# Kernel optimization log

Hardware: AMD Instinct MI355X
Metric: run time of the kernel (lower is better)

The kernel has to match this reference:

```python
import jax, jax.numpy as jnp
import numpy as np

BN_EPS = 1e-5


def _bn(x, gamma, beta):
    # training-mode BatchNorm1d: biased batch stats over the edge/batch axis
    mean = jnp.mean(x, axis=0, keepdims=True)
    var = jnp.mean((x - mean) ** 2, axis=0, keepdims=True)
    return (x - mean) * jax.lax.rsqrt(var + BN_EPS) * gamma + beta


def setup_inputs() -> dict:
    key = jax.random.key(0)
    ks = jax.random.split(key, 20)
    N, E = 20000, 300000
    in_drug, in_prot, hidden = 256, 512, 256
    h2 = 2 * hidden

    def u(k, shape, fan_in):
        b = 1.0 / np.sqrt(fan_in)
        return jax.random.uniform(k, shape, jnp.float32, -b, b)

    return {
        "x_drug": jax.random.normal(ks[0], (N, in_drug), jnp.float32),
        "x_prot": jax.random.normal(ks[1], (N, in_prot), jnp.float32),
        "edge_index": jax.random.randint(ks[2], (2, E), 0, N, jnp.int64),
        "W_src": u(ks[3], (hidden, in_drug), in_drug),
        "W_dst": u(ks[4], (hidden, in_prot), in_prot),
        "W_gate": u(ks[5], (h2, h2), h2),
        "b_gate": u(ks[6], (h2,), h2),
        "W1": u(ks[7], (hidden, h2), h2),
        "b1": u(ks[8], (hidden,), h2),
        "g1": jnp.ones((hidden,), jnp.float32),
        "be1": jnp.zeros((hidden,), jnp.float32),
        "W2": u(ks[9], (hidden, hidden), hidden),
        "b2": u(ks[10], (hidden,), hidden),
        "g2": jnp.ones((hidden,), jnp.float32),
        "be2": jnp.zeros((hidden,), jnp.float32),
        "W3": u(ks[11], (1, hidden), hidden),
        "b3": u(ks[12], (1,), hidden),
        "W_bil": u(ks[13], (1, hidden, hidden), hidden),
        "b_bil": u(ks[14], (1,), hidden),
    }


def reference(x_drug, x_prot, edge_index, W_src, W_dst, W_gate, b_gate,
              W1, b1, g1, be1, W2, b2, g2, be2, W3, b3, W_bil, b_bil):
    src, dst = edge_index[0], edge_index[1]
    h_src = x_drug[src] @ W_src.T            # [E, H]
    h_dst = x_prot[dst] @ W_dst.T            # [E, H]
    h_cat = jnp.concatenate([h_src, h_dst], axis=1)  # [E, 2H]
    gate = jax.nn.sigmoid(h_cat @ W_gate.T + b_gate)
    h = gate * h_cat
    # MLP (dropout is identity here)
    h1 = jax.nn.relu(_bn(h @ W1.T + b1, g1, be1))
    h2_ = jax.nn.relu(_bn(h1 @ W2.T + b2, g2, be2))
    mlp_score = (h2_ @ W3.T + b3).reshape(-1)
    # Bilinear: out_ek = sum_ij h_src_ei W_kij h_dst_ej + b_k
    bil_score = (jnp.einsum("ei,kij,ej->ek", h_src, W_bil, h_dst) + b_bil).reshape(-1)
    return mlp_score + bil_score
```

## Files before the change

### kernel.cpp

```cpp
#include <hip/hip_runtime.h>
#include <hip/hip_bf16.h>

typedef unsigned short u16;
typedef unsigned int u32;
typedef __attribute__((ext_vector_type(8))) short bf16x8;
typedef __attribute__((ext_vector_type(8))) unsigned short us8;
typedef __attribute__((ext_vector_type(4))) float f32x4;


__device__ __forceinline__ float b2f(u16 u) {
    union { unsigned u32v; float f; } x; x.u32v = ((unsigned)u) << 16; return x.f;
}
__device__ __forceinline__ u16 f2b(float f) {
    __hip_bfloat16 h = __float2bfloat16(f);
    u16 r; __builtin_memcpy(&r, &h, 2); return r;
}

struct CvtSeg { const float* in; u16* out; int n4; };
struct CvtArr { CvtSeg s[4]; int tot4; };
__global__ __launch_bounds__(256) void cvt_fused(CvtArr ca) {
    int i = blockIdx.x * 256 + threadIdx.x;
    if (i >= ca.tot4) return;
    int k = 0, off = i;
#pragma unroll
    for (int q = 0; q < 4; ++q) {
        if (off < ca.s[q].n4) { k = q; break; }
        off -= ca.s[q].n4;
    }
    float4 v = ((const float4*)ca.s[k].in)[off];
    ushort4 o; o.x = f2b(v.x); o.y = f2b(v.y); o.z = f2b(v.z); o.w = f2b(v.w);
    ((ushort4*)ca.s[k].out)[off] = o;
}

__global__ __launch_bounds__(256) void repack_swz(const float* __restrict__ W,
                                                  u16* __restrict__ out,
                                                  int total, int kbits) {
    int idx = blockIdx.x * 256 + threadIdx.x;
    if (idx >= total) return;
    const int n = idx >> kbits;
    const int k = idx & ((1 << kbits) - 1);
    const int ks = k >> 6, ke = k & 63;
    const int j = ke ^ ((n & 7) << 3);
    out[(((ks << 8) + n) << 6) + j] = f2b(W[idx]);
}

__global__ __launch_bounds__(256) void hist_kernel(const int* __restrict__ ei,
                                                   int E, u32* __restrict__ hist) {
    int e = blockIdx.x * 256 + threadIdx.x;
    if (e < E) atomicAdd(&hist[ei[E + e]], 1u);
}

__global__ __launch_bounds__(256) void scan_kernel(const u32* __restrict__ hist,
                                                   u32* __restrict__ cursor, int n) {
    __shared__ u32 part[256];
    const int t = threadIdx.x;
    const int chunk = (n + 255) / 256;
    const int lo = t * chunk, hi = min(lo + chunk, n);
    u32 s = 0;
    for (int i = lo; i < hi; ++i) s += hist[i];
    part[t] = s;
    __syncthreads();
    for (int off = 1; off < 256; off <<= 1) {
        u32 v = (t >= off) ? part[t - off] : 0u;
        __syncthreads();
        part[t] += v;
        __syncthreads();
    }
    u32 base = (t == 0) ? 0u : part[t - 1];
    for (int i = lo; i < hi; ++i) {
        cursor[i] = base;
        base += hist[i];
    }
}

__global__ __launch_bounds__(256) void scatter_kernel(const int* __restrict__ ei,
                                                      int E, u32* __restrict__ cursor,
                                                      int2* __restrict__ sd,
                                                      int* __restrict__ pe) {
    int e = blockIdx.x * 256 + threadIdx.x;
    if (e >= E) return;
    const int d = ei[E + e];
    const u32 pos = atomicAdd(&cursor[d], 1u);
    sd[pos] = make_int2(ei[e], d);
    pe[pos] = e;
}

struct GDesc {
    const void* A; int lda; int a_f32;
    const u16* W; int ldb;
    u16* C; int ldc;
    int K;
    const float* bias;
};
template <int NY> struct GDescArr { GDesc d[NY]; };

template <int NY>
__global__ __launch_bounds__(256, 2) void mfma_node(GDescArr<NY> da, int M)
{
    const GDesc dd = da.d[blockIdx.y];
    __shared__ u16 As[2][128][40];
    __shared__ u16 Bs[2][256][40];
    const int t = threadIdx.x;
    const int row0 = blockIdx.x * 128;
    const int arow = t >> 1, aks = (t & 1) * 16;
    const int agr = min(row0 + arow, M - 1);
    const int w = t >> 6, lane = t & 63;
    const int wr = w >> 1, wc = w & 1;
    const int lrow = lane & 15, lkg = lane >> 4;
    const int NIT = dd.K >> 5;

    f32x4 acc[4][8] = {};
    us8 ar[2], br[4];
    float4 fr[4];

    auto load_regs = [&](int it) {
        const int k0 = it << 5;
        if (dd.a_f32) {
            const float* ap = (const float*)dd.A + (size_t)agr * dd.lda + k0 + aks;
#pragma unroll
            for (int q = 0; q < 4; ++q) fr[q] = *(const float4*)(ap + q * 4);
        } else {
            const u16* ap = (const u16*)dd.A + (size_t)agr * dd.lda + k0 + aks;
            ar[0] = *(const us8*)ap; ar[1] = *(const us8*)(ap + 8);
        }
        const u16* wp = dd.W + (size_t)t * dd.ldb + k0;
#pragma unroll
        for (int q = 0; q < 4; ++q) br[q] = *(const us8*)(wp + q * 8);
    };
    auto proc_write = [&](int b) {
        if (dd.a_f32) {
#pragma unroll
            for (int q = 0; q < 2; ++q) {
                us8 o;
                const float fq[8] = {fr[q*2].x, fr[q*2].y, fr[q*2].z, fr[q*2].w,
                                     fr[q*2+1].x, fr[q*2+1].y, fr[q*2+1].z, fr[q*2+1].w};
#pragma unroll
                for (int j = 0; j < 8; ++j) o[j] = f2b(fq[j]);
                *(us8*)&As[b][arow][aks + q * 8] = o;
            }
        } else {
            *(us8*)&As[b][arow][aks] = ar[0];
            *(us8*)&As[b][arow][aks + 8] = ar[1];
        }
#pragma unroll
        for (int q = 0; q < 4; ++q) *(us8*)&Bs[b][t][q * 8] = br[q];
    };
    auto do_mfma = [&](int b) {
        bf16x8 af[4];
#pragma unroll
        for (int mi = 0; mi < 4; ++mi)
            af[mi] = *(const bf16x8*)&As[b][wr * 64 + mi * 16 + lrow][lkg * 8];
#pragma unroll
        for (int ni = 0; ni < 8; ++ni) {
            bf16x8 bfr = *(const bf16x8*)&Bs[b][wc * 128 + ni * 16 + lrow][lkg * 8];
#pragma unroll
            for (int mi = 0; mi < 4; ++mi)
                acc[mi][ni] = __builtin_amdgcn_mfma_f32_16x16x32_bf16(
                    af[mi], bfr, acc[mi][ni], 0, 0, 0);
        }
    };

    load_regs(0); proc_write(0); __syncthreads();
    for (int it = 0; it < NIT; ++it) {
        const int cur = it & 1;
        if (it + 1 < NIT) load_regs(it + 1);
        do_mfma(cur);
        if (it + 1 < NIT) proc_write(cur ^ 1);
        __syncthreads();
    }

#pragma unroll
    for (int ni = 0; ni < 8; ++ni) {
        const int gcol = wc * 128 + ni * 16 + lrow;
        const float bv = dd.bias ? dd.bias[gcol] : 0.f;
#pragma unroll
        for (int mi = 0; mi < 4; ++mi) {
            f32x4 v = acc[mi][ni];
#pragma unroll
            for (int j = 0; j < 4; ++j) {
                const int grow = row0 + wr * 64 + mi * 16 + lkg * 4 + j;
                if (grow < M) dd.C[(size_t)grow * dd.ldc + gcol] = f2b(v[j] + bv);
            }
        }
    }
}

#define OP_GATE   1
#define OP_BNRELU 2

template <int AOP>
__global__ __launch_bounds__(256) void mfma_edge(
    const u16* __restrict__ Ain,
    const u16* __restrict__ Wb, int K,
    u16* __restrict__ C, int E,
    const int2* __restrict__ sd,
    const u16* __restrict__ Gs, const u16* __restrict__ Gd,
    const u16* __restrict__ Hs, const u16* __restrict__ Hd,
    const u16* __restrict__ Bd, const float* __restrict__ b_bil,
    float* __restrict__ bil,
    const float* __restrict__ scaleK, const float* __restrict__ shiftK,
    float* __restrict__ sums)
{
    __shared__ u16 As[64][72];
    __shared__ u16 Bs[256 * 64];
    __shared__ float wsum[2][256];

    const int t = threadIdx.x;
    const int row0 = blockIdx.x * 64;
    const int arow = t >> 2;
    const int aks  = (t & 3) * 16;
    const int agr = min(row0 + arow, E - 1);

    int s_ = 0, d_ = 0;
    if constexpr (AOP == OP_GATE) {
        int2 p = sd[agr]; s_ = p.x; d_ = p.y;
    }

    const int lane = t & 63;
    const int w = t >> 6;
    const int lrow = lane & 15, lkg = lane >> 4;
    const int NKS = K >> 6;

    f32x4 acc[4][4] = {};
    float bdot = 0.f;
    us8 aw0, aw1;

    auto loadA = [&](int ks) {
        const int k = ks * 64 + aks;
        if constexpr (AOP == OP_GATE) {
            us8 gs0 = *(const us8*)(Gs + (size_t)s_ * 512 + k);
            us8 gs1 = *(const us8*)(Gs + (size_t)s_ * 512 + k + 8);
            us8 gd0 = *(const us8*)(Gd + (size_t)d_ * 512 + k);
            us8 gd1 = *(const us8*)(Gd + (size_t)d_ * 512 + k + 8);
            const u16* hp = (ks < 4) ? (Hs + (size_t)s_ * 256 + k)
                                     : (Hd + (size_t)d_ * 256 + k - 256);
            us8 h0 = *(const us8*)hp, h1 = *(const us8*)(hp + 8);
#pragma unroll
            for (int j = 0; j < 8; ++j) {
                const float x0 = b2f(gs0[j]) + b2f(gd0[j]);
                const float x1 = b2f(gs1[j]) + b2f(gd1[j]);
                const float r0 = __builtin_amdgcn_rcpf(1.f + __expf(-x0));
                const float r1 = __builtin_amdgcn_rcpf(1.f + __expf(-x1));
                aw0[j] = f2b(b2f(h0[j]) * r0);
                aw1[j] = f2b(b2f(h1[j]) * r1);
            }
            if (ks < 4) {
                us8 bd0 = *(const us8*)(Bd + (size_t)d_ * 256 + k);
                us8 bd1 = *(const us8*)(Bd + (size_t)d_ * 256 + k + 8);
#pragma unroll
                for (int j = 0; j < 8; ++j) {
                    bdot = fmaf(b2f(h0[j]), b2f(bd0[j]), bdot);
                    bdot = fmaf(b2f(h1[j]), b2f(bd1[j]), bdot);
                }
            }
        } else {
            us8 a0 = *(const us8*)(Ain + (size_t)agr * 256 + k);
            us8 a1 = *(const us8*)(Ain + (size_t)agr * 256 + k + 8);
            float4 c0 = *(const float4*)(scaleK + k);
            float4 c1 = *(const float4*)(scaleK + k + 4);
            float4 c2 = *(const float4*)(scaleK + k + 8);
            float4 c3 = *(const float4*)(scaleK + k + 12);
            float4 h0 = *(const float4*)(shiftK + k);
            float4 h1 = *(const float4*)(shiftK + k + 4);
            float4 h2 = *(const float4*)(shiftK + k + 8);
            float4 h3 = *(const float4*)(shiftK + k + 12);
            const float scq[16] = {c0.x,c0.y,c0.z,c0.w, c1.x,c1.y,c1.z,c1.w,
                                   c2.x,c2.y,c2.z,c2.w, c3.x,c3.y,c3.z,c3.w};
            const float shq[16] = {h0.x,h0.y,h0.z,h0.w, h1.x,h1.y,h1.z,h1.w,
                                   h2.x,h2.y,h2.z,h2.w, h3.x,h3.y,h3.z,h3.w};
#pragma unroll
            for (int j = 0; j < 8; ++j) {
                aw0[j] = f2b(fmaxf(fmaf(b2f(a0[j]), scq[j],     shq[j]),     0.f));
                aw1[j] = f2b(fmaxf(fmaf(b2f(a1[j]), scq[8 + j], shq[8 + j]), 0.f));
            }
        }
    };
    auto writeA = [&]() {
        *(us8*)&As[arow][aks]     = aw0;
        *(us8*)&As[arow][aks + 8] = aw1;
    };
    auto gloadB = [&](int ks) {
        const char* g = (const char*)(Wb + ((size_t)ks << 14)) + w * 8192 + lane * 16;
        char* l = (char*)Bs + w * 8192;
#pragma unroll
        for (int q = 0; q < 8; ++q)
            __builtin_amdgcn_global_load_lds(
                (const __attribute__((address_space(1))) unsigned int*)(g + q * 1024),
                (__attribute__((address_space(3))) unsigned int*)(l + q * 1024),
                16, 0, 0);
    };
    auto mfma_slab = [&]() {
#pragma unroll
        for (int kk = 0; kk < 64; kk += 32) {
            bf16x8 af[4], bf[4];
#pragma unroll
            for (int mi = 0; mi < 4; ++mi)
                af[mi] = *(const bf16x8*)&As[mi * 16 + lrow][kk + lkg * 8];
#pragma unroll
            for (int ni = 0; ni < 4; ++ni) {
                const int r = w * 64 + ni * 16 + lrow;
                bf[ni] = *(const bf16x8*)&Bs[r * 64 + ((kk + lkg * 8) ^ ((r & 7) << 3))];
            }
#pragma unroll
            for (int ni = 0; ni < 4; ++ni)
#pragma unroll
                for (int mi = 0; mi < 4; ++mi)
                    acc[mi][ni] = __builtin_amdgcn_mfma_f32_16x16x32_bf16(
                        af[mi], bf[ni], acc[mi][ni], 0, 0, 0);
        }
    };

    gloadB(0); loadA(0);
    for (int ks = 0; ks < NKS; ++ks) {
        writeA();
        __syncthreads();
        if (ks + 1 < NKS) loadA(ks + 1);
        mfma_slab();
        __syncthreads();
        if (ks + 1 < NKS) gloadB(ks + 1);
    }

    if constexpr (AOP == OP_GATE) {
        bdot += __shfl_xor(bdot, 1, 64);
        bdot += __shfl_xor(bdot, 2, 64);
        if ((t & 3) == 0 && row0 + arow < E)
            bil[row0 + arow] = bdot + b_bil[0];
    }

#pragma unroll
    for (int ni = 0; ni < 4; ++ni) {
        const int gcol = w * 64 + ni * 16 + lrow;
        float s = 0.f, ss = 0.f;
#pragma unroll
        for (int mi = 0; mi < 4; ++mi) {
            f32x4 v = acc[mi][ni];
#pragma unroll
            for (int j = 0; j < 4; ++j) {
                const int grow = row0 + mi * 16 + lkg * 4 + j;
                const float x = v[j];
                if (grow < E) {
                    C[(size_t)grow * 256 + gcol] = f2b(x);
                    s += x; ss = fmaf(x, x, ss);
                }
            }
        }
        s  += __shfl_xor(s, 16, 64);  s  += __shfl_xor(s, 32, 64);
        ss += __shfl_xor(ss, 16, 64); ss += __shfl_xor(ss, 32, 64);
        if (lkg == 0) { wsum[0][gcol] = s; wsum[1][gcol] = ss; }
    }
    __syncthreads();
    atomicAdd(&sums[t],       wsum[0][t]);
    atomicAdd(&sums[256 + t], wsum[1][t]);
}

__global__ void finalize_kernel(
    const float* __restrict__ sums, const float* __restrict__ g,
    const float* __restrict__ be, int M,
    float* __restrict__ scale, float* __restrict__ shift)
{
    const int c = threadIdx.x;
    const float inv = 1.f / (float)M;
    const float mean = sums[c] * inv;
    const float var  = sums[256 + c] * inv - mean * mean;
    const float sc = g[c] * rsqrtf(var + 1e-5f);
    scale[c] = sc;
    shift[c] = fmaf(-mean, sc, be[c]);
}

__global__ __launch_bounds__(256) void final_kernel(
    const u16* __restrict__ Z2,
    const float* __restrict__ scale2, const float* __restrict__ shift2,
    const float* __restrict__ W3, const float* __restrict__ b3,
    const float* __restrict__ bil, const int* __restrict__ pe,
    float* __restrict__ out, int E)
{
    const int w = threadIdx.x >> 6, lane = threadIdx.x & 63;
    const int e = blockIdx.x * 4 + w;
    if (e >= E) return;
    ushort4 zv = *(const ushort4*)(Z2 + (size_t)e * 256 + lane * 4);
    float4 sc = *(const float4*)(scale2 + lane * 4);
    float4 sh = *(const float4*)(shift2 + lane * 4);
    float4 w3 = *(const float4*)(W3 + lane * 4);
    const u16 zq[4] = {zv.x, zv.y, zv.z, zv.w};
    const float scq[4] = {sc.x, sc.y, sc.z, sc.w};
    const float shq[4] = {sh.x, sh.y, sh.z, sh.w};
    const float wq[4] = {w3.x, w3.y, w3.z, w3.w};
    float acc = 0.f;
#pragma unroll
    for (int i = 0; i < 4; ++i) {
        const float x = fmaxf(fmaf(b2f(zq[i]), scq[i], shq[i]), 0.f);
        acc = fmaf(x, wq[i], acc);
    }
#pragma unroll
    for (int off = 32; off; off >>= 1) acc += __shfl_down(acc, off, 64);
    if (lane == 0) out[pe[e]] = acc + b3[0] + bil[e];
}

extern "C" void kernel_launch(void* const* d_in, const int* in_sizes, int n_in,
                              void* d_out, int out_size, void* d_ws, size_t ws_size,
                              hipStream_t stream)
{
    const float* x_drug = (const float*)d_in[0];
    const float* x_prot = (const float*)d_in[1];
    const int*   ei     = (const int*)d_in[2];
    const float* W_src  = (const float*)d_in[3];
    const float* W_dst  = (const float*)d_in[4];
    const float* W_gate = (const float*)d_in[5];
    const float* b_gate = (const float*)d_in[6];
    const float* W1     = (const float*)d_in[7];
    const float* g1     = (const float*)d_in[9];
    const float* be1    = (const float*)d_in[10];
    const float* W2     = (const float*)d_in[11];
    const float* g2     = (const float*)d_in[13];
    const float* be2    = (const float*)d_in[14];
    const float* W3     = (const float*)d_in[15];
    const float* b3     = (const float*)d_in[16];
    const float* W_bil  = (const float*)d_in[17];
    const float* b_bil  = (const float*)d_in[18];
    float* out = (float*)d_out;

    const int N = in_sizes[0] / 256;
    const int E = in_sizes[2] / 2;

    char* wp_ = (char*)d_ws;
    auto alloc = [&](size_t bytes) {
        char* p = wp_; wp_ += (bytes + 255) & ~(size_t)255; return p;
    };
    u16* Wsrcb  = (u16*)alloc(256 * 256 * 2);
    u16* Wdstb  = (u16*)alloc(256 * 512 * 2);
    u16* Wgateb = (u16*)alloc(512 * 512 * 2);
    u16* Wbilb  = (u16*)alloc(256 * 256 * 2);
    u16* W1s    = (u16*)alloc(256 * 512 * 2);
    u16* W2s    = (u16*)alloc(256 * 256 * 2);
    u16* Hs     = (u16*)alloc((size_t)N * 256 * 2);
    u16* Hd     = (u16*)alloc((size_t)N * 256 * 2);
    u16* Gs     = (u16*)alloc((size_t)N * 512 * 2);
    u16* Gd     = (u16*)alloc((size_t)N * 512 * 2);
    u16* Bd     = (u16*)alloc((size_t)N * 256 * 2);
    u16* z      = (u16*)alloc((size_t)E * 256 * 2);
    float* bil  = (float*)alloc((size_t)E * 4);
    u32*  hist  = (u32*)alloc((size_t)N * 4);
    u32*  cursor= (u32*)alloc((size_t)N * 4);
    int2* sd    = (int2*)alloc((size_t)E * 8);
    int*  pe    = (int*)alloc((size_t)E * 4);
    float* sums   = (float*)alloc(1024 * 4);
    float* scale1 = (float*)alloc(256 * 4);
    float* shift1 = (float*)alloc(256 * 4);
    float* scale2 = (float*)alloc(256 * 4);
    float* shift2 = (float*)alloc(256 * 4);

    hipMemsetAsync(sums, 0, 1024 * 4, stream);
    hipMemsetAsync(hist, 0, (size_t)N * 4, stream);

    hist_kernel<<<(E + 255) / 256, 256, 0, stream>>>(ei, E, hist);
    scan_kernel<<<1, 256, 0, stream>>>(hist, cursor, N);
    scatter_kernel<<<(E + 255) / 256, 256, 0, stream>>>(ei, E, cursor, sd, pe);

    CvtArr ca;
    ca.s[0] = {W_src,  Wsrcb,  256 * 256 / 4};
    ca.s[1] = {W_dst,  Wdstb,  256 * 512 / 4};
    ca.s[2] = {W_gate, Wgateb, 512 * 512 / 4};
    ca.s[3] = {W_bil,  Wbilb,  256 * 256 / 4};
    ca.tot4 = 0;
    for (int q = 0; q < 4; ++q) ca.tot4 += ca.s[q].n4;
    cvt_fused<<<(ca.tot4 + 255) / 256, 256, 0, stream>>>(ca);

    repack_swz<<<(256 * 512 + 255) / 256, 256, 0, stream>>>(W1, W1s, 256 * 512, 9);
    repack_swz<<<(256 * 256 + 255) / 256, 256, 0, stream>>>(W2, W2s, 256 * 256, 8);

    const int gxN = (N + 127) / 128;
    const int gxE = (E + 63) / 64;

    GDescArr<2> p1;
    p1.d[0] = {x_drug, 256, 1, Wsrcb, 256, Hs, 256, 256, nullptr};
    p1.d[1] = {x_prot, 512, 1, Wdstb, 512, Hd, 256, 512, nullptr};
    mfma_node<2><<<dim3(gxN, 2), 256, 0, stream>>>(p1, N);

    GDescArr<5> p2;
    p2.d[0] = {Hs, 256, 0, Wgateb,                 512, Gs,       512, 256, b_gate};
    p2.d[1] = {Hs, 256, 0, Wgateb + 256 * 512,     512, Gs + 256, 512, 256, b_gate + 256};
    p2.d[2] = {Hd, 256, 0, Wgateb + 256,           512, Gd,       512, 256, nullptr};
    p2.d[3] = {Hd, 256, 0, Wgateb + 256 * 512 + 256, 512, Gd + 256, 512, 256, nullptr};
    p2.d[4] = {Hd, 256, 0, Wbilb,                  256, Bd,       256, 256, nullptr};
    mfma_node<5><<<dim3(gxN, 5), 256, 0, stream>>>(p2, N);

    mfma_edge<OP_GATE><<<gxE, 256, 0, stream>>>(
        nullptr, W1s, 512, z, E,
        sd, Gs, Gd, Hs, Hd, Bd, b_bil, bil, nullptr, nullptr, sums);
    finalize_kernel<<<1, 256, 0, stream>>>(sums, g1, be1, E, scale1, shift1);

    mfma_edge<OP_BNRELU><<<gxE, 256, 0, stream>>>(
        z, W2s, 256, z, E,
        nullptr, nullptr, nullptr, nullptr, nullptr, nullptr, nullptr, nullptr,
        scale1, shift1, sums + 512);
    finalize_kernel<<<1, 256, 0, stream>>>(sums + 512, g2, be2, E, scale2, shift2);

    final_kernel<<<(E + 3) / 4, 256, 0, stream>>>(
        z, scale2, shift2, W3, b3, bil, pe, out, E);
}
```

Baseline: 564.1 us.

## Split edge A-load into raw load and process, prescale gate by -log2e

The edge GEMM kernel now issues the global loads for the next K-slab before the MFMA work on the current slab. The sigmoid and bias math runs after the MFMAs, so load latency overlaps with matrix compute. The gate node GEMM folds a -log2(e) factor into its output, so the edge kernel can use a raw exp2 instead of __expf. NKS becomes a template parameter so the loop can be fully unrolled. In exchange the kernel holds more live registers for the raw loads, and the bf16 rounding of the prescaled gate logits changes slightly.

```diff
diff --git a/kernel.cpp b/kernel.cpp
--- a/kernel.cpp
+++ b/kernel.cpp
@@ -91,6 +91,7 @@
     u16* C; int ldc;
     int K;
     const float* bias;
+    float cscale;
 };
 template <int NY> struct GDescArr { GDesc d[NY]; };
 
@@ -179,7 +180,8 @@
 #pragma unroll
             for (int j = 0; j < 4; ++j) {
                 const int grow = row0 + wr * 64 + mi * 16 + lkg * 4 + j;
-                if (grow < M) dd.C[(size_t)grow * dd.ldc + gcol] = f2b(v[j] + bv);
+                if (grow < M)
+                    dd.C[(size_t)grow * dd.ldc + gcol] = f2b((v[j] + bv) * dd.cscale);
             }
         }
     }
@@ -188,10 +190,10 @@
 #define OP_GATE   1
 #define OP_BNRELU 2
 
-template <int AOP>
+template <int AOP, int NKS>
 __global__ __launch_bounds__(256) void mfma_edge(
     const u16* __restrict__ Ain,
-    const u16* __restrict__ Wb, int K,
+    const u16* __restrict__ Wb,
     u16* __restrict__ C, int E,
     const int2* __restrict__ sd,
     const u16* __restrict__ Gs, const u16* __restrict__ Gd,
@@ -219,59 +221,67 @@
     const int lane = t & 63;
     const int w = t >> 6;
     const int lrow = lane & 15, lkg = lane >> 4;
-    const int NKS = K >> 6;
 
     f32x4 acc[4][4] = {};
     float bdot = 0.f;
     us8 aw0, aw1;
-
-    auto loadA = [&](int ks) {
+    us8 r0, r1, r2, r3, r4, r5, r6, r7;
+    float4 c0, c1, c2, c3, h0, h1, h2, h3;
+
+    auto rawLoad = [&](int ks) {
         const int k = ks * 64 + aks;
         if constexpr (AOP == OP_GATE) {
-            us8 gs0 = *(const us8*)(Gs + (size_t)s_ * 512 + k);
-            us8 gs1 = *(const us8*)(Gs + (size_t)s_ * 512 + k + 8);
-            us8 gd0 = *(const us8*)(Gd + (size_t)d_ * 512 + k);
-            us8 gd1 = *(const us8*)(Gd + (size_t)d_ * 512 + k + 8);
+            r0 = *(const us8*)(Gs + (size_t)s_ * 512 + k);
+            r1 = *(const us8*)(Gs + (size_t)s_ * 512 + k + 8);
+            r2 = *(const us8*)(Gd + (size_t)d_ * 512 + k);
+            r3 = *(const us8*)(Gd + (size_t)d_ * 512 + k + 8);
             const u16* hp = (ks < 4) ? (Hs + (size_t)s_ * 256 + k)
                                      : (Hd + (size_t)d_ * 256 + k - 256);
-            us8 h0 = *(const us8*)hp, h1 = *(const us8*)(hp + 8);
+            r4 = *(const us8*)hp; r5 = *(const us8*)(hp + 8);
+            if (ks < 4) {
+                r6 = *(const us8*)(Bd + (size_t)d_ * 256 + k);
+                r7 = *(const us8*)(Bd + (size_t)d_ * 256 + k + 8);
+            }
+        } else {
+            r0 = *(const us8*)(Ain + (size_t)agr * 256 + k);
+            r1 = *(const us8*)(Ain + (size_t)agr * 256 + k + 8);
+            c0 = *(const float4*)(scaleK + k);
+            c1 = *(const float4*)(scaleK + k + 4);
+            c2 = *(const float4*)(scaleK + k + 8);
+            c3 = *(const float4*)(scaleK + k + 12);
+            h0 = *(const float4*)(shiftK + k);
+            h1 = *(const float4*)(shiftK + k + 4);
+            h2 = *(const float4*)(shiftK + k + 8);
+            h3 = *(const float4*)(shiftK + k + 12);
+        }
+    };
+    auto proc = [&](int ks) {
+        if constexpr (AOP == OP_GATE) {
 #pragma unroll
             for (int j = 0; j < 8; ++j) {
-                const float x0 = b2f(gs0[j]) + b2f(gd0[j]);
-                const float x1 = b2f(gs1[j]) + b2f(gd1[j]);
-                const float r0 = __builtin_amdgcn_rcpf(1.f + __expf(-x0));
-                const float r1 = __builtin_amdgcn_rcpf(1.f + __expf(-x1));
-                aw0[j] = f2b(b2f(h0[j]) * r0);
-                aw1[j] = f2b(b2f(h1[j]) * r1);
+                const float x0 = b2f(r0[j]) + b2f(r2[j]);
+                const float x1 = b2f(r1[j]) + b2f(r3[j]);
+                const float g0 = __builtin_amdgcn_rcpf(1.f + __builtin_amdgcn_exp2f(x0));
+                const float g1 = __builtin_amdgcn_rcpf(1.f + __builtin_amdgcn_exp2f(x1));
+                aw0[j] = f2b(b2f(r4[j]) * g0);
+                aw1[j] = f2b(b2f(r5[j]) * g1);
             }
             if (ks < 4) {
-                us8 bd0 = *(const us8*)(Bd + (size_t)d_ * 256 + k);
-                us8 bd1 = *(const us8*)(Bd + (size_t)d_ * 256 + k + 8);
 #pragma unroll
                 for (int j = 0; j < 8; ++j) {
-                    bdot = fmaf(b2f(h0[j]), b2f(bd0[j]), bdot);
-                    bdot = fmaf(b2f(h1[j]), b2f(bd1[j]), bdot);
+                    bdot = fmaf(b2f(r4[j]), b2f(r6[j]), bdot);
+                    bdot = fmaf(b2f(r5[j]), b2f(r7[j]), bdot);
                 }
             }
         } else {
-            us8 a0 = *(const us8*)(Ain + (size_t)agr * 256 + k);
-            us8 a1 = *(const us8*)(Ain + (size_t)agr * 256 + k + 8);
-            float4 c0 = *(const float4*)(scaleK + k);
-            float4 c1 = *(const float4*)(scaleK + k + 4);
-            float4 c2 = *(const float4*)(scaleK + k + 8);
-            float4 c3 = *(const float4*)(scaleK + k + 12);
-            float4 h0 = *(const float4*)(shiftK + k);
-            float4 h1 = *(const float4*)(shiftK + k + 4);
-            float4 h2 = *(const float4*)(shiftK + k + 8);
-            float4 h3 = *(const float4*)(shiftK + k + 12);
             const float scq[16] = {c0.x,c0.y,c0.z,c0.w, c1.x,c1.y,c1.z,c1.w,
                                    c2.x,c2.y,c2.z,c2.w, c3.x,c3.y,c3.z,c3.w};
             const float shq[16] = {h0.x,h0.y,h0.z,h0.w, h1.x,h1.y,h1.z,h1.w,
                                    h2.x,h2.y,h2.z,h2.w, h3.x,h3.y,h3.z,h3.w};
 #pragma unroll
             for (int j = 0; j < 8; ++j) {
-                aw0[j] = f2b(fmaxf(fmaf(b2f(a0[j]), scq[j],     shq[j]),     0.f));
-                aw1[j] = f2b(fmaxf(fmaf(b2f(a1[j]), scq[8 + j], shq[8 + j]), 0.f));
+                aw0[j] = f2b(fmaxf(fmaf(b2f(r0[j]), scq[j],     shq[j]),     0.f));
+                aw1[j] = f2b(fmaxf(fmaf(b2f(r1[j]), scq[8 + j], shq[8 + j]), 0.f));
             }
         }
     };
@@ -310,14 +320,20 @@
         }
     };
 
-    gloadB(0); loadA(0);
+    rawLoad(0); gloadB(0);
+    proc(0); writeA();
+    __syncthreads();
+#pragma unroll
     for (int ks = 0; ks < NKS; ++ks) {
-        writeA();
-        __syncthreads();
-        if (ks + 1 < NKS) loadA(ks + 1);
+        if (ks + 1 < NKS) rawLoad(ks + 1);
         mfma_slab();
-        __syncthreads();
-        if (ks + 1 < NKS) gloadB(ks + 1);
+        if (ks + 1 < NKS) {
+            proc(ks + 1);
+            __syncthreads();
+            writeA();
+            gloadB(ks + 1);
+            __syncthreads();
+        }
     }
 
     if constexpr (AOP == OP_GATE) {
@@ -421,6 +437,7 @@
 
     const int N = in_sizes[0] / 256;
     const int E = in_sizes[2] / 2;
+    const float NL2E = -1.4426950408889634f;
 
     char* wp_ = (char*)d_ws;
     auto alloc = [&](size_t bytes) {
@@ -472,25 +489,25 @@
     const int gxE = (E + 63) / 64;
 
     GDescArr<2> p1;
-    p1.d[0] = {x_drug, 256, 1, Wsrcb, 256, Hs, 256, 256, nullptr};
-    p1.d[1] = {x_prot, 512, 1, Wdstb, 512, Hd, 256, 512, nullptr};
+    p1.d[0] = {x_drug, 256, 1, Wsrcb, 256, Hs, 256, 256, nullptr, 1.f};
+    p1.d[1] = {x_prot, 512, 1, Wdstb, 512, Hd, 256, 512, nullptr, 1.f};
     mfma_node<2><<<dim3(gxN, 2), 256, 0, stream>>>(p1, N);
 
     GDescArr<5> p2;
-    p2.d[0] = {Hs, 256, 0, Wgateb,                 512, Gs,       512, 256, b_gate};
-    p2.d[1] = {Hs, 256, 0, Wgateb + 256 * 512,     512, Gs + 256, 512, 256, b_gate + 256};
-    p2.d[2] = {Hd, 256, 0, Wgateb + 256,           512, Gd,       512, 256, nullptr};
-    p2.d[3] = {Hd, 256, 0, Wgateb + 256 * 512 + 256, 512, Gd + 256, 512, 256, nullptr};
-    p2.d[4] = {Hd, 256, 0, Wbilb,                  256, Bd,       256, 256, nullptr};
+    p2.d[0] = {Hs, 256, 0, Wgateb,                 512, Gs,       512, 256, b_gate,       NL2E};
+    p2.d[1] = {Hs, 256, 0, Wgateb + 256 * 512,     512, Gs + 256, 512, 256, b_gate + 256, NL2E};
+    p2.d[2] = {Hd, 256, 0, Wgateb + 256,           512, Gd,       512, 256, nullptr,      NL2E};
+    p2.d[3] = {Hd, 256, 0, Wgateb + 256 * 512 + 256, 512, Gd + 256, 512, 256, nullptr,    NL2E};
+    p2.d[4] = {Hd, 256, 0, Wbilb,                  256, Bd,       256, 256, nullptr,      1.f};
     mfma_node<5><<<dim3(gxN, 5), 256, 0, stream>>>(p2, N);
 
-    mfma_edge<OP_GATE><<<gxE, 256, 0, stream>>>(
-        nullptr, W1s, 512, z, E,
+    mfma_edge<OP_GATE, 8><<<gxE, 256, 0, stream>>>(
+        nullptr, W1s, z, E,
         sd, Gs, Gd, Hs, Hd, Bd, b_bil, bil, nullptr, nullptr, sums);
     finalize_kernel<<<1, 256, 0, stream>>>(sums, g1, be1, E, scale1, shift1);
 
-    mfma_edge<OP_BNRELU><<<gxE, 256, 0, stream>>>(
-        z, W2s, 256, z, E,
+    mfma_edge<OP_BNRELU, 4><<<gxE, 256, 0, stream>>>(
+        z, W2s, z, E,
         nullptr, nullptr, nullptr, nullptr, nullptr, nullptr, nullptr, nullptr,
         scale1, shift1, sums + 512);
     finalize_kernel<<<1, 256, 0, stream>>>(sums + 512, g2, be2, E, scale2, shift2);
```

Result: slower. 596.0 us (+5.7%).

## Double edge-kernel block size to 512 threads with narrower per-wave tiles

Applied to the files above, without the earlier changes.

The edge MFMA kernels now launch 512 threads per 64-row block. Each of the 8 waves computes 32 output columns instead of 64, and each thread gathers and processes 8 A elements per k-slab instead of 16. The A-operand load is also split into a separate load phase and a processing phase. The aim is more waves in flight to hide the latency of the random gathers and the sigmoid math. In exchange, each wave reuses its A fragments across fewer B columns, there is more LDS traffic per MFMA, and barriers now span twice as many waves.

```diff
diff --git a/kernel.cpp b/kernel.cpp
--- a/kernel.cpp
+++ b/kernel.cpp
@@ -189,7 +189,7 @@
 #define OP_BNRELU 2
 
 template <int AOP>
-__global__ __launch_bounds__(256) void mfma_edge(
+__global__ __launch_bounds__(512) void mfma_edge(
     const u16* __restrict__ Ain,
     const u16* __restrict__ Wb, int K,
     u16* __restrict__ C, int E,
@@ -207,8 +207,8 @@
 
     const int t = threadIdx.x;
     const int row0 = blockIdx.x * 64;
-    const int arow = t >> 2;
-    const int aks  = (t & 3) * 16;
+    const int arow = t >> 3;
+    const int aks  = (t & 7) * 8;
     const int agr = min(row0 + arow, E - 1);
 
     int s_ = 0, d_ = 0;
@@ -221,69 +221,58 @@
     const int lrow = lane & 15, lkg = lane >> 4;
     const int NKS = K >> 6;
 
-    f32x4 acc[4][4] = {};
+    f32x4 acc[4][2] = {};
     float bdot = 0.f;
-    us8 aw0, aw1;
+    us8 aw0;
+    us8 r0, r1, r2, r3;
+    float4 c0, c1, h0, h1;
 
     auto loadA = [&](int ks) {
         const int k = ks * 64 + aks;
         if constexpr (AOP == OP_GATE) {
-            us8 gs0 = *(const us8*)(Gs + (size_t)s_ * 512 + k);
-            us8 gs1 = *(const us8*)(Gs + (size_t)s_ * 512 + k + 8);
-            us8 gd0 = *(const us8*)(Gd + (size_t)d_ * 512 + k);
-            us8 gd1 = *(const us8*)(Gd + (size_t)d_ * 512 + k + 8);
+            r0 = *(const us8*)(Gs + (size_t)s_ * 512 + k);
+            r1 = *(const us8*)(Gd + (size_t)d_ * 512 + k);
             const u16* hp = (ks < 4) ? (Hs + (size_t)s_ * 256 + k)
                                      : (Hd + (size_t)d_ * 256 + k - 256);
-            us8 h0 = *(const us8*)hp, h1 = *(const us8*)(hp + 8);
+            r2 = *(const us8*)hp;
+            if (ks < 4) r3 = *(const us8*)(Bd + (size_t)d_ * 256 + k);
+        } else {
+            r0 = *(const us8*)(Ain + (size_t)agr * 256 + k);
+            c0 = *(const float4*)(scaleK + k);
+            c1 = *(const float4*)(scaleK + k + 4);
+            h0 = *(const float4*)(shiftK + k);
+            h1 = *(const float4*)(shiftK + k + 4);
+        }
+    };
+    auto proc = [&](int ks) {
+        if constexpr (AOP == OP_GATE) {
 #pragma unroll
             for (int j = 0; j < 8; ++j) {
-                const float x0 = b2f(gs0[j]) + b2f(gd0[j]);
-                const float x1 = b2f(gs1[j]) + b2f(gd1[j]);
-                const float r0 = __builtin_amdgcn_rcpf(1.f + __expf(-x0));
-                const float r1 = __builtin_amdgcn_rcpf(1.f + __expf(-x1));
-                aw0[j] = f2b(b2f(h0[j]) * r0);
-                aw1[j] = f2b(b2f(h1[j]) * r1);
+                const float x = b2f(r0[j]) + b2f(r1[j]);
+                const float g = __builtin_amdgcn_rcpf(1.f + __expf(-x));
+                aw0[j] = f2b(b2f(r2[j]) * g);
             }
             if (ks < 4) {
-                us8 bd0 = *(const us8*)(Bd + (size_t)d_ * 256 + k);
-                us8 bd1 = *(const us8*)(Bd + (size_t)d_ * 256 + k + 8);
-#pragma unroll
-                for (int j = 0; j < 8; ++j) {
-                    bdot = fmaf(b2f(h0[j]), b2f(bd0[j]), bdot);
-                    bdot = fmaf(b2f(h1[j]), b2f(bd1[j]), bdot);
-                }
+#pragma unroll
+                for (int j = 0; j < 8; ++j)
+                    bdot = fmaf(b2f(r2[j]), b2f(r3[j]), bdot);
             }
         } else {
-            us8 a0 = *(const us8*)(Ain + (size_t)agr * 256 + k);
-            us8 a1 = *(const us8*)(Ain + (size_t)agr * 256 + k + 8);
-            float4 c0 = *(const float4*)(scaleK + k);
-            float4 c1 = *(const float4*)(scaleK + k + 4);
-            float4 c2 = *(const float4*)(scaleK + k + 8);
-            float4 c3 = *(const float4*)(scaleK + k + 12);
-            float4 h0 = *(const float4*)(shiftK + k);
-            float4 h1 = *(const float4*)(shiftK + k + 4);
-            float4 h2 = *(const float4*)(shiftK + k + 8);
-            float4 h3 = *(const float4*)(shiftK + k + 12);
-            const float scq[16] = {c0.x,c0.y,c0.z,c0.w, c1.x,c1.y,c1.z,c1.w,
-                                   c2.x,c2.y,c2.z,c2.w, c3.x,c3.y,c3.z,c3.w};
-            const float shq[16] = {h0.x,h0.y,h0.z,h0.w, h1.x,h1.y,h1.z,h1.w,
-                                   h2.x,h2.y,h2.z,h2.w, h3.x,h3.y,h3.z,h3.w};
-#pragma unroll
-            for (int j = 0; j < 8; ++j) {
-                aw0[j] = f2b(fmaxf(fmaf(b2f(a0[j]), scq[j],     shq[j]),     0.f));
-                aw1[j] = f2b(fmaxf(fmaf(b2f(a1[j]), scq[8 + j], shq[8 + j]), 0.f));
-            }
+            const float scq[8] = {c0.x,c0.y,c0.z,c0.w, c1.x,c1.y,c1.z,c1.w};
+            const float shq[8] = {h0.x,h0.y,h0.z,h0.w, h1.x,h1.y,h1.z,h1.w};
+#pragma unroll
+            for (int j = 0; j < 8; ++j)
+                aw0[j] = f2b(fmaxf(fmaf(b2f(r0[j]), scq[j], shq[j]), 0.f));
         }
     };
     auto writeA = [&]() {
-        *(us8*)&As[arow][aks]     = aw0;
-        *(us8*)&As[arow][aks + 8] = aw1;
+        *(us8*)&As[arow][aks] = aw0;
     };
     auto gloadB = [&](int ks) {
-        const char* g = (const char*)(Wb + ((size_t)ks << 14)) + w * 8192 + lane * 16;
-        char* l = (char*)Bs + w * 8192;
-#pragma unroll
-        for (int q = 0; q < 8; ++q)
+        const char* g = (const char*)(Wb + ((size_t)ks << 14)) + w * 4096 + lane * 16;
+        char* l = (char*)Bs + w * 4096;
+#pragma unroll
+        for (int q = 0; q < 4; ++q)
             __builtin_amdgcn_global_load_lds(
                 (const __attribute__((address_space(1))) unsigned int*)(g + q * 1024),
                 (__attribute__((address_space(3))) unsigned int*)(l + q * 1024),
@@ -292,17 +281,17 @@
     auto mfma_slab = [&]() {
 #pragma unroll
         for (int kk = 0; kk < 64; kk += 32) {
-            bf16x8 af[4], bf[4];
+            bf16x8 af[4], bf[2];
 #pragma unroll
             for (int mi = 0; mi < 4; ++mi)
                 af[mi] = *(const bf16x8*)&As[mi * 16 + lrow][kk + lkg * 8];
 #pragma unroll
-            for (int ni = 0; ni < 4; ++ni) {
-                const int r = w * 64 + ni * 16 + lrow;
+            for (int ni = 0; ni < 2; ++ni) {
+                const int r = w * 32 + ni * 16 + lrow;
                 bf[ni] = *(const bf16x8*)&Bs[r * 64 + ((kk + lkg * 8) ^ ((r & 7) << 3))];
             }
 #pragma unroll
-            for (int ni = 0; ni < 4; ++ni)
+            for (int ni = 0; ni < 2; ++ni)
 #pragma unroll
                 for (int mi = 0; mi < 4; ++mi)
                     acc[mi][ni] = __builtin_amdgcn_mfma_f32_16x16x32_bf16(
@@ -310,11 +299,11 @@
         }
     };
 
-    gloadB(0); loadA(0);
+    gloadB(0); loadA(0); proc(0);
     for (int ks = 0; ks < NKS; ++ks) {
         writeA();
         __syncthreads();
-        if (ks + 1 < NKS) loadA(ks + 1);
+        if (ks + 1 < NKS) { loadA(ks + 1); proc(ks + 1); }
         mfma_slab();
         __syncthreads();
         if (ks + 1 < NKS) gloadB(ks + 1);
@@ -323,13 +312,14 @@
     if constexpr (AOP == OP_GATE) {
         bdot += __shfl_xor(bdot, 1, 64);
         bdot += __shfl_xor(bdot, 2, 64);
-        if ((t & 3) == 0 && row0 + arow < E)
+        bdot += __shfl_xor(bdot, 4, 64);
+        if ((t & 7) == 0 && row0 + arow < E)
             bil[row0 + arow] = bdot + b_bil[0];
     }
 
 #pragma unroll
-    for (int ni = 0; ni < 4; ++ni) {
-        const int gcol = w * 64 + ni * 16 + lrow;
+    for (int ni = 0; ni < 2; ++ni) {
+        const int gcol = w * 32 + ni * 16 + lrow;
         float s = 0.f, ss = 0.f;
 #pragma unroll
         for (int mi = 0; mi < 4; ++mi) {
@@ -349,8 +339,10 @@
         if (lkg == 0) { wsum[0][gcol] = s; wsum[1][gcol] = ss; }
     }
     __syncthreads();
-    atomicAdd(&sums[t],       wsum[0][t]);
-    atomicAdd(&sums[256 + t], wsum[1][t]);
+    if (t < 256) {
+        atomicAdd(&sums[t],       wsum[0][t]);
+        atomicAdd(&sums[256 + t], wsum[1][t]);
+    }
 }
 
 __global__ void finalize_kernel(
@@ -484,12 +476,12 @@
     p2.d[4] = {Hd, 256, 0, Wbilb,                  256, Bd,       256, 256, nullptr};
     mfma_node<5><<<dim3(gxN, 5), 256, 0, stream>>>(p2, N);
 
-    mfma_edge<OP_GATE><<<gxE, 256, 0, stream>>>(
+    mfma_edge<OP_GATE><<<gxE, 512, 0, stream>>>(
         nullptr, W1s, 512, z, E,
         sd, Gs, Gd, Hs, Hd, Bd, b_bil, bil, nullptr, nullptr, sums);
     finalize_kernel<<<1, 256, 0, stream>>>(sums, g1, be1, E, scale1, shift1);
 
-    mfma_edge<OP_BNRELU><<<gxE, 256, 0, stream>>>(
+    mfma_edge<OP_BNRELU><<<gxE, 512, 0, stream>>>(
         z, W2s, 256, z, E,
         nullptr, nullptr, nullptr, nullptr, nullptr, nullptr, nullptr, nullptr,
         scale1, shift1, sums + 512);
```

Result: slower. 586.3 us (+3.9%).
